# Optimization experiments

Hardware: AMD Instinct MI355X
Metric: run time of the kernel (lower is better)

## Reference

```python
import jax, jax.numpy as jnp
import numpy as np

B, X, C = 8192, 8, 512        # batch, map_num, img_dim==tex_dim
P, Y = 8, 1000                # n_prompts, cls_num
FAKE = 16                     # fake prompt width (hardcoded in module)
F = 2048                      # feat_dim
CLS = 1000                    # cls_num
IN_DIM = P * X * FAKE         # 1024
SF = 64.0


def setup_inputs() -> dict:
    key = jax.random.key(0)
    ks = jax.random.split(key, 8)
    s = 0.02
    return {
        "img_f": jax.random.normal(ks[0], (B, X, C), jnp.float32),
        "tex_f": jax.random.normal(ks[1], (P, Y, C), jnp.float32),
        "fake_cls": jax.random.normal(ks[2], (P, FAKE, C), jnp.float32),
        "fc_w": jax.random.normal(ks[3], (C, C), jnp.float32) * s,
        "fc_b": jnp.zeros((C,), jnp.float32),
        "bn1_g": jnp.ones((IN_DIM,), jnp.float32),
        "bn1_b": jnp.zeros((IN_DIM,), jnp.float32),
        "w1": jax.random.normal(ks[4], (F, IN_DIM), jnp.float32) * s,
        "b1": jnp.zeros((F,), jnp.float32),
        "bn2_g": jnp.ones((F,), jnp.float32),
        "bn2_b": jnp.zeros((F,), jnp.float32),
        "w2": jax.random.normal(ks[5], (CLS, F), jnp.float32) * s,
        "b2": jnp.zeros((CLS,), jnp.float32),
    }


def _bn(x, g, b, eps=1e-5):
    # BatchNorm1d in training mode: batch mean / biased batch var
    m = x.mean(axis=0)
    v = x.var(axis=0)
    return (x - m) * jax.lax.rsqrt(v + eps) * g + b


def reference(img_f, tex_f, fake_cls, fc_w, fc_b, bn1_g, bn1_b, w1, b1,
              bn2_g, bn2_b, w2, b2):
    # independent L2 norm over feature dim, scaled by x_sf=64
    img_n = img_f / (jnp.linalg.norm(img_f, axis=-1, keepdims=True) + 1e-6) * SF
    tex_n = tex_f / (jnp.linalg.norm(tex_f, axis=-1, keepdims=True) + 1e-6) * SF
    # prompt attention over the class axis
    tex_fc = jnp.einsum('pyc,dc->pyd', tex_n, fc_w) + fc_b          # fc(tex_f)
    attn = jax.nn.softmax(jnp.einsum('pxc,pyc->pxy', fake_cls, tex_fc), axis=-1)
    tex_a = jnp.einsum('pxy,pyc->pxc', attn, tex_n)                  # (P,16,C)
    # cross-modal relation: 'b x c, y d c -> b yxd' (icomp/tcomp are Identity)
    cp = jnp.einsum('bxc,pdc->bpxd', img_n, tex_a).reshape(img_n.shape[0], -1)
    # prt_fc: BN -> Linear -> ELU -> BN -> Linear
    h = jax.nn.elu(_bn(cp, bn1_g, bn1_b) @ w1.T + b1)
    return _bn(h, bn2_g, bn2_b) @ w2.T + b2
```

## Files before the change

### kernel.cpp

```cpp
#include <hip/hip_runtime.h>
#include <math.h>


typedef __attribute__((ext_vector_type(8))) short bf16x8;
typedef __attribute__((ext_vector_type(4))) float f32x4;

__device__ __forceinline__ float waveSum(float v) {
#pragma unroll
    for (int o = 32; o > 0; o >>= 1) v += __shfl_xor(v, o);
    return v;
}
__device__ __forceinline__ float waveMax(float v) {
#pragma unroll
    for (int o = 32; o > 0; o >>= 1) v = fmaxf(v, __shfl_xor(v, o));
    return v;
}
__device__ __forceinline__ unsigned short f2bf(float x) {
    union { float f; unsigned u; } v; v.f = x;
    unsigned r = v.u + 0x7FFFu + ((v.u >> 16) & 1u);
    return (unsigned short)(r >> 16);
}
__device__ __forceinline__ float bf2f(unsigned short h) {
    union { unsigned u; float f; } v; v.u = ((unsigned)h) << 16; return v.f;
}
__device__ __forceinline__ void gload16(const void* g, const void* l) {
    __builtin_amdgcn_global_load_lds((const __attribute__((address_space(1))) void*)g,
                                     (__attribute__((address_space(3))) void*)l, 16, 0, 0);
}
__device__ __forceinline__ int xcd_swz(int d, int n) {
    int q = n >> 3;
    return (d & 7) * q + (d >> 3);
}

__global__ __launch_bounds__(256) void k_rownorm_bf(const float* __restrict__ in,
                                                    unsigned short* __restrict__ out) {
    int row = blockIdx.x, t = threadIdx.x;
    const float* r = in + (size_t)row * 512;
    float2 v = *(const float2*)(r + t * 2);
    float ss = v.x * v.x + v.y * v.y;
    ss = waveSum(ss);
    __shared__ float sred[4];
    if ((t & 63) == 0) sred[t >> 6] = ss;
    __syncthreads();
    float tot = sred[0] + sred[1] + sred[2] + sred[3];
    float sc = 64.f / (sqrtf(tot) + 1e-6f);
    unsigned u = (unsigned)f2bf(v.x * sc) | ((unsigned)f2bf(v.y * sc) << 16);
    *(unsigned*)(out + (size_t)row * 512 + t * 2) = u;
}

__global__ __launch_bounds__(256) void k_imgnorm(const float* __restrict__ in,
                                                 float* __restrict__ inv) {
    int row = blockIdx.x * 4 + (threadIdx.x >> 6);
    int lane = threadIdx.x & 63;
    const float* r = in + (size_t)row * 512 + lane * 8;
    float4 a = *(const float4*)r;
    float4 b = *(const float4*)(r + 4);
    float ss = a.x*a.x + a.y*a.y + a.z*a.z + a.w*a.w
             + b.x*b.x + b.y*b.y + b.z*b.z + b.w*b.w;
    ss = waveSum(ss);
    if (lane == 0) inv[row] = 64.f / (sqrtf(ss) + 1e-6f);
}

__global__ __launch_bounds__(256) void k_gbf(const float* __restrict__ fake_cls,
                                             const float* __restrict__ fc_w,
                                             unsigned short* __restrict__ g_bf) {
    int bid = blockIdx.x, t = threadIdx.x;
    __shared__ float fcls[512];
    fcls[t]       = fake_cls[bid * 512 + t];
    fcls[t + 256] = fake_cls[bid * 512 + t + 256];
    __syncthreads();
    float a0 = 0.f, a1 = 0.f;
    for (int d = 0; d < 512; ++d) {
        float fv = fcls[d];
        a0 = fmaf(fv, fc_w[d * 512 + t], a0);
        a1 = fmaf(fv, fc_w[d * 512 + t + 256], a1);
    }
    g_bf[bid * 512 + t]       = f2bf(a0);
    g_bf[bid * 512 + t + 256] = f2bf(a1);
}

__global__ __launch_bounds__(256) void k_softmax(const float* __restrict__ logits,
                                                 unsigned short* __restrict__ attnw) {
    int row = blockIdx.x, t = threadIdx.x, lane = t & 63, wid = t >> 6;
    __shared__ float sred[4];
    float v[4];
#pragma unroll
    for (int i = 0; i < 4; ++i) {
        int y = t + i * 256;
        v[i] = (y < 1000) ? logits[(size_t)row * 1000 + y] : -3.0e38f;
    }
    float m = fmaxf(fmaxf(v[0], v[1]), fmaxf(v[2], v[3]));
    m = waveMax(m);
    if (lane == 0) sred[wid] = m;
    __syncthreads();
    m = fmaxf(fmaxf(sred[0], sred[1]), fmaxf(sred[2], sred[3]));
    __syncthreads();
    float s = 0.f;
#pragma unroll
    for (int i = 0; i < 4; ++i) {
        int y = t + i * 256;
        float e = (y < 1000) ? expf(v[i] - m) : 0.f;
        v[i] = e;
        s += e;
    }
    s = waveSum(s);
    if (lane == 0) sred[wid] = s;
    __syncthreads();
    float inv = 1.f / (sred[0] + sred[1] + sred[2] + sred[3]);
#pragma unroll
    for (int i = 0; i < 4; ++i)
        attnw[(size_t)row * 1024 + t + i * 256] = f2bf(v[i] * inv);
}

__global__ __launch_bounds__(256) void k_wsum(const unsigned short* __restrict__ attnw,
                                              const unsigned short* __restrict__ texn,
                                              float* __restrict__ part) {
    int yt = blockIdx.x, p = blockIdx.y, t = threadIdx.x;
    __shared__ float wl[16][125];
    for (int idx = t; idx < 16 * 125; idx += 256) {
        int x = idx / 125, y = idx % 125;
        wl[x][y] = bf2f(attnw[(size_t)(p * 16 + x) * 1024 + yt * 125 + y]);
    }
    __syncthreads();
    int c0 = t * 2;
    const unsigned short* tp = texn + ((size_t)p * 1000 + yt * 125) * 512 + c0;
    float a0[16], a1[16];
#pragma unroll
    for (int x = 0; x < 16; ++x) { a0[x] = 0.f; a1[x] = 0.f; }
    for (int y = 0; y < 125; ++y) {
        unsigned u = *(const unsigned*)(tp + (size_t)y * 512);
        float lo = bf2f((unsigned short)(u & 0xffff));
        float hi = bf2f((unsigned short)(u >> 16));
#pragma unroll
        for (int x = 0; x < 16; ++x) {
            float w = wl[x][y];
            a0[x] = fmaf(w, lo, a0[x]);
            a1[x] = fmaf(w, hi, a1[x]);
        }
    }
#pragma unroll
    for (int x = 0; x < 16; ++x) {
        float* dst = part + ((size_t)((p * 8 + yt) * 16 + x)) * 512 + c0;
        dst[0] = a0[x];
        dst[1] = a1[x];
    }
}

__global__ __launch_bounds__(256) void k_texa_red(const float* __restrict__ part,
                                                  unsigned short* __restrict__ texa) {
    int row = blockIdx.x, t = threadIdx.x;
    int p = row >> 4, x = row & 15;
    int c = t * 2;
    float s0 = 0.f, s1 = 0.f;
#pragma unroll
    for (int yt = 0; yt < 8; ++yt) {
        const float* src = part + ((size_t)((p * 8 + yt) * 16 + x)) * 512 + c;
        s0 += src[0];
        s1 += src[1];
    }
    unsigned u = (unsigned)f2bf(s0) | ((unsigned)f2bf(s1) << 16);
    *(unsigned*)(texa + (size_t)row * 512 + c) = u;
}

__global__ __launch_bounds__(256) void k_colstat_bf(const unsigned short* __restrict__ src,
                                                    float* __restrict__ ps,
                                                    float* __restrict__ pq, int ncols) {
    int col = blockIdx.x * 256 + threadIdx.x;
    int r0 = blockIdx.y * 128;
    const unsigned short* p = src + (size_t)r0 * ncols + col;
    float s = 0.f, q = 0.f;
    for (int r = 0; r < 128; ++r) {
        float v = bf2f(p[(size_t)r * ncols]);
        s += v;
        q = fmaf(v, v, q);
    }
    ps[(size_t)blockIdx.y * ncols + col] = s;
    pq[(size_t)blockIdx.y * ncols + col] = q;
}

template <bool PERM>
__global__ __launch_bounds__(256) void k_bnfin(const float* __restrict__ ps,
                                               const float* __restrict__ pq,
                                               const float* __restrict__ gam,
                                               const float* __restrict__ bet,
                                               float* __restrict__ a, float* __restrict__ c,
                                               int ncols) {
    int col = blockIdx.x * 256 + threadIdx.x;
    float S = 0.f, Q = 0.f;
    for (int i = 0; i < 64; ++i) {
        S += ps[(size_t)i * ncols + col];
        Q += pq[(size_t)i * ncols + col];
    }
    float mean = S * (1.f / 8192.f);
    float var = Q * (1.f / 8192.f) - mean * mean;
    int j = col;
    if (PERM) {
        int x = col >> 7, jj = col & 127, pp = jj >> 4, d = jj & 15;
        j = (pp << 7) + (x << 4) + d;
    }
    float av = gam[j] * rsqrtf(var + 1e-5f);
    a[col] = av;
    c[col] = bet[j] - mean * av;
}

template <bool PERM>
__global__ __launch_bounds__(256) void k_foldw_bf(const float* __restrict__ W,
                                                  const float* __restrict__ bin,
                                                  const float* __restrict__ a,
                                                  const float* __restrict__ c,
                                                  unsigned short* __restrict__ Wout,
                                                  float* __restrict__ bout,
                                                  int Kdim, int nvalid) {
    int f = blockIdx.x, t = threadIdx.x;
    unsigned short* wo = Wout + (size_t)f * Kdim;
    if (f >= nvalid) {
        for (int col = t; col < Kdim; col += 256) wo[col] = 0;
        if (t == 0) bout[f] = 0.f;
        return;
    }
    const float* wr = W + (size_t)f * Kdim;
    float partial = 0.f;
    for (int col = t; col < Kdim; col += 256) {
        int j = col;
        if (PERM) {
            int x = col >> 7, jj = col & 127, pp = jj >> 4, d = jj & 15;
            j = (pp << 7) + (x << 4) + d;
        }
        float wv = wr[j];
        wo[col] = f2bf(wv * a[col]);
        partial = fmaf(wv, c[col], partial);
    }
    partial = waveSum(partial);
    __shared__ float sred[4];
    if ((t & 63) == 0) sred[t >> 6] = partial;
    __syncthreads();
    if (t == 0) bout[f] = bin[f] + sred[0] + sred[1] + sred[2] + sred[3];
}

template <int EPI, bool A_F32>
__global__ __launch_bounds__(256) void gemm_mfma(const void* __restrict__ Av,
                                                 const unsigned short* __restrict__ Bv,
                                                 void* __restrict__ Cv, int K,
                                                 int ntn, int ldc, int nvalid,
                                                 const float* __restrict__ rowscale,
                                                 const float* __restrict__ bias,
                                                 int aZ, int bZ, int cZ) {
    __shared__ unsigned short Asl[128 * 64];
    __shared__ unsigned short Bsl[128 * 64];
    const int tid = threadIdx.x;
    const int lane = tid & 63, wid = tid >> 6;
    const int wr = wid >> 1, wc = wid & 1;
    const int wg = xcd_swz(blockIdx.x, gridDim.x);
    const int m0 = (wg / ntn) * 128, n0 = (wg % ntn) * 128;
    const int z = blockIdx.y;

    const float* Af = (const float*)Av;
    const unsigned short* Ab = (const unsigned short*)Av + (size_t)z * aZ;
    const unsigned short* B = Bv + (size_t)z * bZ;

    f32x4 acc[4][4];
#pragma unroll
    for (int i = 0; i < 4; ++i)
#pragma unroll
        for (int j = 0; j < 4; ++j) acc[i][j] = {0.f, 0.f, 0.f, 0.f};

    const int swz = ((lane & 7) ^ (lane >> 3)) * 8;
    const int lrow = lane & 15, lkh = lane >> 4;

    for (int k0 = 0; k0 < K; k0 += 64) {
        if (A_F32) {
#pragma unroll
            for (int r = 0; r < 4; ++r) {
                int row = r * 32 + (tid >> 3);
                int kk = (tid & 7) * 8;
                const float* src = Af + (size_t)(m0 + row) * K + k0 + kk;
                float4 p0 = *(const float4*)src;
                float4 p1 = *(const float4*)(src + 4);
                float sc = rowscale[m0 + row];
                bf16x8 v;
                v[0] = (short)f2bf(p0.x * sc); v[1] = (short)f2bf(p0.y * sc);
                v[2] = (short)f2bf(p0.z * sc); v[3] = (short)f2bf(p0.w * sc);
                v[4] = (short)f2bf(p1.x * sc); v[5] = (short)f2bf(p1.y * sc);
                v[6] = (short)f2bf(p1.z * sc); v[7] = (short)f2bf(p1.w * sc);
                *(bf16x8*)&Asl[row * 64 + (kk ^ ((row & 7) << 3))] = v;
            }
        } else {
#pragma unroll
            for (int r = 0; r < 4; ++r) {
                int row = r * 32 + wid * 8 + (lane >> 3);
                gload16(Ab + (size_t)(m0 + row) * K + k0 + swz,
                        Asl + r * 2048 + wid * 512);
            }
        }
#pragma unroll
        for (int r = 0; r < 4; ++r) {
            int row = r * 32 + wid * 8 + (lane >> 3);
            gload16(B + (size_t)(n0 + row) * K + k0 + swz,
                    Bsl + r * 2048 + wid * 512);
        }
        __syncthreads();
#pragma unroll
        for (int kk = 0; kk < 2; ++kk) {
            bf16x8 af[4], bfr[4];
#pragma unroll
            for (int m = 0; m < 4; ++m) {
                int row = wr * 64 + m * 16 + lrow;
                af[m] = *(const bf16x8*)&Asl[row * 64 + ((kk * 32 + lkh * 8) ^ ((row & 7) << 3))];
            }
#pragma unroll
            for (int n = 0; n < 4; ++n) {
                int row = wc * 64 + n * 16 + lrow;
                bfr[n] = *(const bf16x8*)&Bsl[row * 64 + ((kk * 32 + lkh * 8) ^ ((row & 7) << 3))];
            }
#pragma unroll
            for (int m = 0; m < 4; ++m)
#pragma unroll
                for (int n = 0; n < 4; ++n)
                    acc[m][n] = __builtin_amdgcn_mfma_f32_16x16x32_bf16(af[m], bfr[n], acc[m][n], 0, 0, 0);
        }
        __syncthreads();
    }

    const int colbase = n0 + wc * 64 + lrow;
    float bv[4];
    if (EPI == 1 || EPI == 2) {
#pragma unroll
        for (int n = 0; n < 4; ++n) bv[n] = bias[colbase + n * 16];
    }
    if (EPI == 0 || EPI == 1) {
        unsigned short* C = (unsigned short*)Cv;
#pragma unroll
        for (int m = 0; m < 4; ++m) {
            int row = m0 + wr * 64 + m * 16 + lkh * 4;
#pragma unroll
            for (int r = 0; r < 4; ++r)
#pragma unroll
                for (int n = 0; n < 4; ++n) {
                    float v = acc[m][n][r];
                    if (EPI == 1) {
                        v += bv[n];
                        v = v > 0.f ? v : expm1f(v);
                    }
                    C[(size_t)(row + r) * ldc + colbase + n * 16] = f2bf(v);
                }
        }
    } else {
        float* C = (float*)Cv + (size_t)z * cZ;
#pragma unroll
        for (int m = 0; m < 4; ++m) {
            int row = m0 + wr * 64 + m * 16 + lkh * 4;
#pragma unroll
            for (int r = 0; r < 4; ++r) {
                if (EPI == 3 && (row + r) >= 16) continue;
#pragma unroll
                for (int n = 0; n < 4; ++n) {
                    int col = colbase + n * 16;
                    if (col < nvalid) {
                        float v = acc[m][n][r];
                        if (EPI == 2) v += bv[n];
                        C[(size_t)(row + r) * ldc + col] = v;
                    }
                }
            }
        }
    }
}

extern "C" void kernel_launch(void* const* d_in, const int* in_sizes, int n_in,
                              void* d_out, int out_size, void* d_ws, size_t ws_size,
                              hipStream_t stream) {
    const float* img_f    = (const float*)d_in[0];
    const float* tex_f    = (const float*)d_in[1];
    const float* fake_cls = (const float*)d_in[2];
    const float* fc_w     = (const float*)d_in[3];
    const float* bn1_g    = (const float*)d_in[5];
    const float* bn1_b    = (const float*)d_in[6];
    const float* w1       = (const float*)d_in[7];
    const float* b1       = (const float*)d_in[8];
    const float* bn2_g    = (const float*)d_in[9];
    const float* bn2_b    = (const float*)d_in[10];
    const float* w2       = (const float*)d_in[11];
    const float* b2       = (const float*)d_in[12];
    float* out = (float*)d_out;

    char* w = (char*)d_ws;
    unsigned short* texn = (unsigned short*)(w);
    unsigned short* g_bf = (unsigned short*)(w + 8388608);
    float*          logit= (float*)(w + 8650752);
    unsigned short* attnw= (unsigned short*)(w + 9175040);
    float*          part = (float*)(w + 9437184);
    unsigned short* texa = (unsigned short*)(w + 11534336);
    float*          inv  = (float*)(w + 11665408);
    unsigned short* cp   = (unsigned short*)(w + 11927552);
    unsigned short* w1a  = (unsigned short*)(w + 28704768);
    float*          b1p  = (float*)(w + 32899072);
    float*          a1   = (float*)(w + 32907264);
    float*          c1   = (float*)(w + 32911360);
    float*          ps   = (float*)(w + 32915456);
    float*          pq   = (float*)(w + 33439744);
    unsigned short* h    = (unsigned short*)(w + 33964032);
    unsigned short* w2a  = (unsigned short*)(w + 67518464);
    float*          b2p  = (float*)(w + 71712768);
    float*          a2   = (float*)(w + 71716864);
    float*          c2   = (float*)(w + 71725056);

    k_rownorm_bf<<<8000, 256, 0, stream>>>(tex_f, texn);
    k_imgnorm<<<16384, 256, 0, stream>>>(img_f, inv);
    k_gbf<<<128, 256, 0, stream>>>(fake_cls, fc_w, g_bf);
    gemm_mfma<3, false><<<dim3(8, 8), 256, 0, stream>>>(
        g_bf, texn, logit, 512, 8, 1000, 1000, nullptr, nullptr,
        16 * 512, 1000 * 512, 16 * 1000);
    k_softmax<<<128, 256, 0, stream>>>(logit, attnw);
    k_wsum<<<dim3(8, 8), 256, 0, stream>>>(attnw, texn, part);
    k_texa_red<<<128, 256, 0, stream>>>(part, texa);

    gemm_mfma<0, true><<<dim3(512, 1), 256, 0, stream>>>(
        img_f, texa, cp, 512, 1, 128, 128, inv, nullptr, 0, 0, 0);

    k_colstat_bf<<<dim3(4, 64), 256, 0, stream>>>(cp, ps, pq, 1024);
    k_bnfin<true><<<4, 256, 0, stream>>>(ps, pq, bn1_g, bn1_b, a1, c1, 1024);
    k_foldw_bf<true><<<2048, 256, 0, stream>>>(w1, b1, a1, c1, w1a, b1p, 1024, 2048);

    gemm_mfma<1, false><<<dim3(1024, 1), 256, 0, stream>>>(
        cp, w1a, h, 1024, 16, 2048, 2048, nullptr, b1p, 0, 0, 0);

    k_colstat_bf<<<dim3(8, 64), 256, 0, stream>>>(h, ps, pq, 2048);
    k_bnfin<false><<<8, 256, 0, stream>>>(ps, pq, bn2_g, bn2_b, a2, c2, 2048);
    k_foldw_bf<false><<<1024, 256, 0, stream>>>(w2, b2, a2, c2, w2a, b2p, 2048, 1000);

    gemm_mfma<2, false><<<dim3(512, 1), 256, 0, stream>>>(
        h, w2a, out, 2048, 8, 1000, 1000, nullptr, b2p, 0, 0, 0);
}
```

Measured before the change: 277.1 us.

## Fuse norms, softmax, and BN2 column stats into neighboring kernels

Merges the tex row-norm and fake_cls·fc_w kernels into one launch. Folds the softmax into the attention-weighted sum kernel, which now uses 16 y-tiles. Drops the separate img row-norm pass: the first GEMM accumulates row sums of squares while staging A and applies the inverse norm in its epilogue. The h GEMM now writes per-tile column sums and squared sums, removing the separate column-stats read of h. This cuts launches and a full re-read of the 8192x8x512 img_f input and the large h matrix. The cost is redundant softmax max/sum work in every y-tile block, and BN2 stats now come from bf16-unrounded ELU values over 128-row tiles, where the k_bnfin reduction must match that tile count.

```diff
diff --git a/kernel.cpp b/kernel.cpp
--- a/kernel.cpp
+++ b/kernel.cpp
@@ -32,115 +32,87 @@
     return (d & 7) * q + (d >> 3);
 }
 
-__global__ __launch_bounds__(256) void k_rownorm_bf(const float* __restrict__ in,
-                                                    unsigned short* __restrict__ out) {
-    int row = blockIdx.x, t = threadIdx.x;
-    const float* r = in + (size_t)row * 512;
-    float2 v = *(const float2*)(r + t * 2);
-    float ss = v.x * v.x + v.y * v.y;
-    ss = waveSum(ss);
+__global__ __launch_bounds__(256) void k_prep(const float* __restrict__ tex_f,
+                                              unsigned short* __restrict__ texn,
+                                              const float* __restrict__ fake_cls,
+                                              const float* __restrict__ fc_w,
+                                              unsigned short* __restrict__ g_bf) {
     __shared__ float sred[4];
-    if ((t & 63) == 0) sred[t >> 6] = ss;
+    __shared__ float fcls[512];
+    int bid = blockIdx.x, t = threadIdx.x;
+    if (bid < 8000) {
+        const float* r = tex_f + (size_t)bid * 512;
+        float2 v = *(const float2*)(r + t * 2);
+        float ss = v.x * v.x + v.y * v.y;
+        ss = waveSum(ss);
+        if ((t & 63) == 0) sred[t >> 6] = ss;
+        __syncthreads();
+        float tot = sred[0] + sred[1] + sred[2] + sred[3];
+        float sc = 64.f / (sqrtf(tot) + 1e-6f);
+        unsigned u = (unsigned)f2bf(v.x * sc) | ((unsigned)f2bf(v.y * sc) << 16);
+        *(unsigned*)(texn + (size_t)bid * 512 + t * 2) = u;
+    } else {
+        int row = bid - 8000;
+        fcls[t]       = fake_cls[row * 512 + t];
+        fcls[t + 256] = fake_cls[row * 512 + t + 256];
+        __syncthreads();
+        float a0 = 0.f, a1 = 0.f;
+        for (int d = 0; d < 512; ++d) {
+            float fv = fcls[d];
+            a0 = fmaf(fv, fc_w[d * 512 + t], a0);
+            a1 = fmaf(fv, fc_w[d * 512 + t + 256], a1);
+        }
+        g_bf[row * 512 + t]       = f2bf(a0);
+        g_bf[row * 512 + t + 256] = f2bf(a1);
+    }
+}
+
+__global__ __launch_bounds__(256) void k_wsum_sm(const float* __restrict__ logit,
+                                                 const unsigned short* __restrict__ texn,
+                                                 float* __restrict__ part) {
+    int yt = blockIdx.x, p = blockIdx.y, t = threadIdx.x;
+    int lane = t & 63, w = t >> 6;
+    __shared__ float wl[16][63];
+    __shared__ float ms[16], iss[16];
+    const int y0 = yt * 63;
+    const int ylen = min(63, 1000 - y0);
+#pragma unroll
+    for (int rr = 0; rr < 4; ++rr) {
+        int x = w * 4 + rr;
+        const float* lr = logit + ((size_t)p * 16 + x) * 1000;
+        float m = -3.0e38f;
+        for (int y = lane; y < 1000; y += 64) m = fmaxf(m, lr[y]);
+        m = waveMax(m);
+        float s = 0.f;
+        for (int y = lane; y < 1000; y += 64) s += expf(lr[y] - m);
+        s = waveSum(s);
+        if (lane == 0) { ms[x] = m; iss[x] = 1.f / s; }
+    }
     __syncthreads();
-    float tot = sred[0] + sred[1] + sred[2] + sred[3];
-    float sc = 64.f / (sqrtf(tot) + 1e-6f);
-    unsigned u = (unsigned)f2bf(v.x * sc) | ((unsigned)f2bf(v.y * sc) << 16);
-    *(unsigned*)(out + (size_t)row * 512 + t * 2) = u;
-}
-
-__global__ __launch_bounds__(256) void k_imgnorm(const float* __restrict__ in,
-                                                 float* __restrict__ inv) {
-    int row = blockIdx.x * 4 + (threadIdx.x >> 6);
-    int lane = threadIdx.x & 63;
-    const float* r = in + (size_t)row * 512 + lane * 8;
-    float4 a = *(const float4*)r;
-    float4 b = *(const float4*)(r + 4);
-    float ss = a.x*a.x + a.y*a.y + a.z*a.z + a.w*a.w
-             + b.x*b.x + b.y*b.y + b.z*b.z + b.w*b.w;
-    ss = waveSum(ss);
-    if (lane == 0) inv[row] = 64.f / (sqrtf(ss) + 1e-6f);
-}
-
-__global__ __launch_bounds__(256) void k_gbf(const float* __restrict__ fake_cls,
-                                             const float* __restrict__ fc_w,
-                                             unsigned short* __restrict__ g_bf) {
-    int bid = blockIdx.x, t = threadIdx.x;
-    __shared__ float fcls[512];
-    fcls[t]       = fake_cls[bid * 512 + t];
-    fcls[t + 256] = fake_cls[bid * 512 + t + 256];
-    __syncthreads();
-    float a0 = 0.f, a1 = 0.f;
-    for (int d = 0; d < 512; ++d) {
-        float fv = fcls[d];
-        a0 = fmaf(fv, fc_w[d * 512 + t], a0);
-        a1 = fmaf(fv, fc_w[d * 512 + t + 256], a1);
-    }
-    g_bf[bid * 512 + t]       = f2bf(a0);
-    g_bf[bid * 512 + t + 256] = f2bf(a1);
-}
-
-__global__ __launch_bounds__(256) void k_softmax(const float* __restrict__ logits,
-                                                 unsigned short* __restrict__ attnw) {
-    int row = blockIdx.x, t = threadIdx.x, lane = t & 63, wid = t >> 6;
-    __shared__ float sred[4];
-    float v[4];
-#pragma unroll
-    for (int i = 0; i < 4; ++i) {
-        int y = t + i * 256;
-        v[i] = (y < 1000) ? logits[(size_t)row * 1000 + y] : -3.0e38f;
-    }
-    float m = fmaxf(fmaxf(v[0], v[1]), fmaxf(v[2], v[3]));
-    m = waveMax(m);
-    if (lane == 0) sred[wid] = m;
-    __syncthreads();
-    m = fmaxf(fmaxf(sred[0], sred[1]), fmaxf(sred[2], sred[3]));
-    __syncthreads();
-    float s = 0.f;
-#pragma unroll
-    for (int i = 0; i < 4; ++i) {
-        int y = t + i * 256;
-        float e = (y < 1000) ? expf(v[i] - m) : 0.f;
-        v[i] = e;
-        s += e;
-    }
-    s = waveSum(s);
-    if (lane == 0) sred[wid] = s;
-    __syncthreads();
-    float inv = 1.f / (sred[0] + sred[1] + sred[2] + sred[3]);
-#pragma unroll
-    for (int i = 0; i < 4; ++i)
-        attnw[(size_t)row * 1024 + t + i * 256] = f2bf(v[i] * inv);
-}
-
-__global__ __launch_bounds__(256) void k_wsum(const unsigned short* __restrict__ attnw,
-                                              const unsigned short* __restrict__ texn,
-                                              float* __restrict__ part) {
-    int yt = blockIdx.x, p = blockIdx.y, t = threadIdx.x;
-    __shared__ float wl[16][125];
-    for (int idx = t; idx < 16 * 125; idx += 256) {
-        int x = idx / 125, y = idx % 125;
-        wl[x][y] = bf2f(attnw[(size_t)(p * 16 + x) * 1024 + yt * 125 + y]);
+    for (int idx = t; idx < 16 * ylen; idx += 256) {
+        int x = idx / ylen, y = idx % ylen;
+        wl[x][y] = expf(logit[((size_t)p * 16 + x) * 1000 + y0 + y] - ms[x]) * iss[x];
     }
     __syncthreads();
     int c0 = t * 2;
-    const unsigned short* tp = texn + ((size_t)p * 1000 + yt * 125) * 512 + c0;
+    const unsigned short* tp = texn + ((size_t)p * 1000 + y0) * 512 + c0;
     float a0[16], a1[16];
 #pragma unroll
     for (int x = 0; x < 16; ++x) { a0[x] = 0.f; a1[x] = 0.f; }
-    for (int y = 0; y < 125; ++y) {
+    for (int y = 0; y < ylen; ++y) {
         unsigned u = *(const unsigned*)(tp + (size_t)y * 512);
         float lo = bf2f((unsigned short)(u & 0xffff));
         float hi = bf2f((unsigned short)(u >> 16));
 #pragma unroll
         for (int x = 0; x < 16; ++x) {
-            float w = wl[x][y];
-            a0[x] = fmaf(w, lo, a0[x]);
-            a1[x] = fmaf(w, hi, a1[x]);
+            float ww = wl[x][y];
+            a0[x] = fmaf(ww, lo, a0[x]);
+            a1[x] = fmaf(ww, hi, a1[x]);
         }
     }
 #pragma unroll
     for (int x = 0; x < 16; ++x) {
-        float* dst = part + ((size_t)((p * 8 + yt) * 16 + x)) * 512 + c0;
+        float* dst = part + ((size_t)((yt * 8 + p) * 16 + x)) * 512 + c0;
         dst[0] = a0[x];
         dst[1] = a1[x];
     }
@@ -153,8 +125,8 @@
     int c = t * 2;
     float s0 = 0.f, s1 = 0.f;
 #pragma unroll
-    for (int yt = 0; yt < 8; ++yt) {
-        const float* src = part + ((size_t)((p * 8 + yt) * 16 + x)) * 512 + c;
+    for (int yt = 0; yt < 16; ++yt) {
+        const float* src = part + ((size_t)((yt * 8 + p) * 16 + x)) * 512 + c;
         s0 += src[0];
         s1 += src[1];
     }
@@ -237,16 +209,19 @@
     if (t == 0) bout[f] = bin[f] + sred[0] + sred[1] + sred[2] + sred[3];
 }
 
-template <int EPI, bool A_F32>
+template <int EPI, bool A_F32, bool STATS>
 __global__ __launch_bounds__(256) void gemm_mfma(const void* __restrict__ Av,
                                                  const unsigned short* __restrict__ Bv,
                                                  void* __restrict__ Cv, int K,
                                                  int ntn, int ldc, int nvalid,
-                                                 const float* __restrict__ rowscale,
                                                  const float* __restrict__ bias,
+                                                 float* __restrict__ ps,
+                                                 float* __restrict__ pq,
                                                  int aZ, int bZ, int cZ) {
     __shared__ unsigned short Asl[128 * 64];
     __shared__ unsigned short Bsl[128 * 64];
+    __shared__ float extraA[128];
+    __shared__ float extraB[128];
     const int tid = threadIdx.x;
     const int lane = tid & 63, wid = tid >> 6;
     const int wr = wid >> 1, wc = wid & 1;
@@ -266,6 +241,7 @@
 
     const int swz = ((lane & 7) ^ (lane >> 3)) * 8;
     const int lrow = lane & 15, lkh = lane >> 4;
+    float ssq[4] = {0.f, 0.f, 0.f, 0.f};
 
     for (int k0 = 0; k0 < K; k0 += 64) {
         if (A_F32) {
@@ -276,12 +252,13 @@
                 const float* src = Af + (size_t)(m0 + row) * K + k0 + kk;
                 float4 p0 = *(const float4*)src;
                 float4 p1 = *(const float4*)(src + 4);
-                float sc = rowscale[m0 + row];
+                ssq[r] += p0.x*p0.x + p0.y*p0.y + p0.z*p0.z + p0.w*p0.w
+                        + p1.x*p1.x + p1.y*p1.y + p1.z*p1.z + p1.w*p1.w;
                 bf16x8 v;
-                v[0] = (short)f2bf(p0.x * sc); v[1] = (short)f2bf(p0.y * sc);
-                v[2] = (short)f2bf(p0.z * sc); v[3] = (short)f2bf(p0.w * sc);
-                v[4] = (short)f2bf(p1.x * sc); v[5] = (short)f2bf(p1.y * sc);
-                v[6] = (short)f2bf(p1.z * sc); v[7] = (short)f2bf(p1.w * sc);
+                v[0] = (short)f2bf(p0.x); v[1] = (short)f2bf(p0.y);
+                v[2] = (short)f2bf(p0.z); v[3] = (short)f2bf(p0.w);
+                v[4] = (short)f2bf(p1.x); v[5] = (short)f2bf(p1.y);
+                v[6] = (short)f2bf(p1.z); v[7] = (short)f2bf(p1.w);
                 *(bf16x8*)&Asl[row * 64 + (kk ^ ((row & 7) << 3))] = v;
             }
         } else {
@@ -321,14 +298,38 @@
         __syncthreads();
     }
 
+    if (A_F32) {
+#pragma unroll
+        for (int r = 0; r < 4; ++r) {
+            float s = ssq[r];
+            s += __shfl_xor(s, 1); s += __shfl_xor(s, 2); s += __shfl_xor(s, 4);
+            if ((tid & 7) == 0) extraA[r * 32 + (tid >> 3)] = 64.f / (sqrtf(s) + 1e-6f);
+        }
+        __syncthreads();
+    }
+
     const int colbase = n0 + wc * 64 + lrow;
     float bv[4];
     if (EPI == 1 || EPI == 2) {
 #pragma unroll
         for (int n = 0; n < 4; ++n) bv[n] = bias[colbase + n * 16];
     }
-    if (EPI == 0 || EPI == 1) {
+    if (EPI == 0) {
         unsigned short* C = (unsigned short*)Cv;
+#pragma unroll
+        for (int m = 0; m < 4; ++m) {
+            int rloc = wr * 64 + m * 16 + lkh * 4;
+#pragma unroll
+            for (int r = 0; r < 4; ++r) {
+                float riv = extraA[rloc + r];
+#pragma unroll
+                for (int n = 0; n < 4; ++n)
+                    C[(size_t)(m0 + rloc + r) * ldc + colbase + n * 16] = f2bf(acc[m][n][r] * riv);
+            }
+        }
+    } else if (EPI == 1) {
+        unsigned short* C = (unsigned short*)Cv;
+        float sN[4] = {0.f, 0.f, 0.f, 0.f}, qN[4] = {0.f, 0.f, 0.f, 0.f};
 #pragma unroll
         for (int m = 0; m < 4; ++m) {
             int row = m0 + wr * 64 + m * 16 + lkh * 4;
@@ -336,13 +337,41 @@
             for (int r = 0; r < 4; ++r)
 #pragma unroll
                 for (int n = 0; n < 4; ++n) {
-                    float v = acc[m][n][r];
-                    if (EPI == 1) {
-                        v += bv[n];
-                        v = v > 0.f ? v : expm1f(v);
-                    }
+                    float v = acc[m][n][r] + bv[n];
+                    v = v > 0.f ? v : expm1f(v);
+                    sN[n] += v;
+                    qN[n] = fmaf(v, v, qN[n]);
                     C[(size_t)(row + r) * ldc + colbase + n * 16] = f2bf(v);
                 }
+        }
+        if (STATS) {
+#pragma unroll
+            for (int n = 0; n < 4; ++n) {
+                sN[n] += __shfl_xor(sN[n], 16); sN[n] += __shfl_xor(sN[n], 32);
+                qN[n] += __shfl_xor(qN[n], 16); qN[n] += __shfl_xor(qN[n], 32);
+            }
+            __syncthreads();
+            if (wr == 0 && lane < 16) {
+#pragma unroll
+                for (int n = 0; n < 4; ++n) {
+                    extraA[wc * 64 + n * 16 + lrow] = sN[n];
+                    extraB[wc * 64 + n * 16 + lrow] = qN[n];
+                }
+            }
+            __syncthreads();
+            if (wr == 1 && lane < 16) {
+#pragma unroll
+                for (int n = 0; n < 4; ++n) {
+                    extraA[wc * 64 + n * 16 + lrow] += sN[n];
+                    extraB[wc * 64 + n * 16 + lrow] += qN[n];
+                }
+            }
+            __syncthreads();
+            if (tid < 128) {
+                int mt = wg / ntn;
+                ps[(size_t)mt * ldc + n0 + tid] = extraA[tid];
+                pq[(size_t)mt * ldc + n0 + tid] = extraB[tid];
+            }
         }
     } else {
         float* C = (float*)Cv + (size_t)z * cZ;
@@ -387,47 +416,41 @@
     unsigned short* texn = (unsigned short*)(w);
     unsigned short* g_bf = (unsigned short*)(w + 8388608);
     float*          logit= (float*)(w + 8650752);
-    unsigned short* attnw= (unsigned short*)(w + 9175040);
-    float*          part = (float*)(w + 9437184);
-    unsigned short* texa = (unsigned short*)(w + 11534336);
-    float*          inv  = (float*)(w + 11665408);
-    unsigned short* cp   = (unsigned short*)(w + 11927552);
-    unsigned short* w1a  = (unsigned short*)(w + 28704768);
-    float*          b1p  = (float*)(w + 32899072);
-    float*          a1   = (float*)(w + 32907264);
-    float*          c1   = (float*)(w + 32911360);
-    float*          ps   = (float*)(w + 32915456);
-    float*          pq   = (float*)(w + 33439744);
-    unsigned short* h    = (unsigned short*)(w + 33964032);
-    unsigned short* w2a  = (unsigned short*)(w + 67518464);
-    float*          b2p  = (float*)(w + 71712768);
-    float*          a2   = (float*)(w + 71716864);
-    float*          c2   = (float*)(w + 71725056);
-
-    k_rownorm_bf<<<8000, 256, 0, stream>>>(tex_f, texn);
-    k_imgnorm<<<16384, 256, 0, stream>>>(img_f, inv);
-    k_gbf<<<128, 256, 0, stream>>>(fake_cls, fc_w, g_bf);
-    gemm_mfma<3, false><<<dim3(8, 8), 256, 0, stream>>>(
-        g_bf, texn, logit, 512, 8, 1000, 1000, nullptr, nullptr,
+    float*          part = (float*)(w + 9175040);
+    unsigned short* texa = (unsigned short*)(w + 13369344);
+    unsigned short* cp   = (unsigned short*)(w + 13500416);
+    unsigned short* w1a  = (unsigned short*)(w + 30277632);
+    float*          b1p  = (float*)(w + 34471936);
+    float*          a1   = (float*)(w + 34480128);
+    float*          c1   = (float*)(w + 34484224);
+    float*          ps   = (float*)(w + 34488320);
+    float*          pq   = (float*)(w + 35012608);
+    unsigned short* h    = (unsigned short*)(w + 35536896);
+    unsigned short* w2a  = (unsigned short*)(w + 69091328);
+    float*          b2p  = (float*)(w + 73285632);
+    float*          a2   = (float*)(w + 73289728);
+    float*          c2   = (float*)(w + 73297920);
+
+    k_prep<<<8128, 256, 0, stream>>>(tex_f, texn, fake_cls, fc_w, g_bf);
+    gemm_mfma<3, false, false><<<dim3(8, 8), 256, 0, stream>>>(
+        g_bf, texn, logit, 512, 8, 1000, 1000, nullptr, nullptr, nullptr,
         16 * 512, 1000 * 512, 16 * 1000);
-    k_softmax<<<128, 256, 0, stream>>>(logit, attnw);
-    k_wsum<<<dim3(8, 8), 256, 0, stream>>>(attnw, texn, part);
+    k_wsum_sm<<<dim3(16, 8), 256, 0, stream>>>(logit, texn, part);
     k_texa_red<<<128, 256, 0, stream>>>(part, texa);
 
-    gemm_mfma<0, true><<<dim3(512, 1), 256, 0, stream>>>(
-        img_f, texa, cp, 512, 1, 128, 128, inv, nullptr, 0, 0, 0);
+    gemm_mfma<0, true, false><<<dim3(512, 1), 256, 0, stream>>>(
+        img_f, texa, cp, 512, 1, 128, 128, nullptr, nullptr, nullptr, 0, 0, 0);
 
     k_colstat_bf<<<dim3(4, 64), 256, 0, stream>>>(cp, ps, pq, 1024);
     k_bnfin<true><<<4, 256, 0, stream>>>(ps, pq, bn1_g, bn1_b, a1, c1, 1024);
     k_foldw_bf<true><<<2048, 256, 0, stream>>>(w1, b1, a1, c1, w1a, b1p, 1024, 2048);
 
-    gemm_mfma<1, false><<<dim3(1024, 1), 256, 0, stream>>>(
-        cp, w1a, h, 1024, 16, 2048, 2048, nullptr, b1p, 0, 0, 0);
-
-    k_colstat_bf<<<dim3(8, 64), 256, 0, stream>>>(h, ps, pq, 2048);
+    gemm_mfma<1, false, true><<<dim3(1024, 1), 256, 0, stream>>>(
+        cp, w1a, h, 1024, 16, 2048, 2048, b1p, ps, pq, 0, 0, 0);
+
     k_bnfin<false><<<8, 256, 0, stream>>>(ps, pq, bn2_g, bn2_b, a2, c2, 2048);
     k_foldw_bf<false><<<1024, 256, 0, stream>>>(w2, b2, a2, c2, w2a, b2p, 2048, 1000);
 
-    gemm_mfma<2, false><<<dim3(512, 1), 256, 0, stream>>>(
-        h, w2a, out, 2048, 8, 1000, 1000, nullptr, b2p, 0, 0, 0);
-}
+    gemm_mfma<2, false, false><<<dim3(512, 1), 256, 0, stream>>>(
+        h, w2a, out, 2048, 8, 1000, 1000, b2p, nullptr, nullptr, 0, 0, 0);
+}
```

Result: faster. 249.7 us (-9.9%).
